# Optimization experiments

Hardware: AMD Instinct MI355X
Metric: run time of the kernel (lower is better)

## Reference

```python
import jax, jax.numpy as jnp
import numpy as np

H = 1024  # hidden size

def lstm_cell(x, h, c, Wih, Whh, b):
    # torch gate order: i, f, g, o
    g = x @ Wih.T + h @ Whh.T + b
    i, f, gg, o = jnp.split(g, 4, axis=-1)
    c = jax.nn.sigmoid(f) * c + jax.nn.sigmoid(i) * jnp.tanh(gg)
    h = jax.nn.sigmoid(o) * jnp.tanh(c)
    return h, c

def lstm_layer(x, Wih, Whh, b):
    # x: [B, S, in] -> (y [B, S, H], h_last [B, H], c_last [B, H])
    B = x.shape[0]
    h0 = jnp.zeros((B, H), x.dtype)
    def step(carry, xt):
        h, c = carry
        h, c = lstm_cell(xt, h, c, Wih, Whh, b)
        return (h, c), h
    (h, c), ys = jax.lax.scan(step, (h0, h0), jnp.swapaxes(x, 0, 1))
    return jnp.swapaxes(ys, 0, 1), h, c

def setup_inputs() -> dict:
    key = jax.random.key(0)
    ks = iter(jax.random.split(key, 24))
    V, E, B, Ss, St = 32000, 512, 32, 64, 64
    s = 0.05
    d = {
        'source': jax.random.randint(next(ks), (B, Ss), 0, V),
        'prev_outputs': jax.random.randint(next(ks), (B, St), 0, V),
        'emb': jax.random.normal(next(ks), (V, E)) * s,
        'enc_Wih0': jax.random.normal(next(ks), (4*H, E)) * s,
        'enc_Whh0': jax.random.normal(next(ks), (4*H, H)) * s,
        'enc_b0': jax.random.normal(next(ks), (4*H,)) * s,
        'enc_Wih1': jax.random.normal(next(ks), (4*H, H)) * s,
        'enc_Whh1': jax.random.normal(next(ks), (4*H, H)) * s,
        'enc_b1': jax.random.normal(next(ks), (4*H,)) * s,
        'dec_Wih0': jax.random.normal(next(ks), (4*H, E + H)) * s,
        'dec_Whh0': jax.random.normal(next(ks), (4*H, H)) * s,
        'dec_b0': jax.random.normal(next(ks), (4*H,)) * s,
        'dec_Wih1': jax.random.normal(next(ks), (4*H, H)) * s,
        'dec_Whh1': jax.random.normal(next(ks), (4*H, H)) * s,
        'dec_b1': jax.random.normal(next(ks), (4*H,)) * s,
        'Wk': jax.random.normal(next(ks), (H, H)) * s,
        'bk': jax.random.normal(next(ks), (H,)) * s,
        'Wh': jax.random.normal(next(ks), (V, H)) * s,
        'bh': jax.random.normal(next(ks), (V,)) * s,
    }
    return d

def reference(source, prev_outputs, emb, enc_Wih0, enc_Whh0, enc_b0,
              enc_Wih1, enc_Whh1, enc_b1, dec_Wih0, dec_Whh0, dec_b0,
              dec_Wih1, dec_Whh1, dec_b1, Wk, bk, Wh, bh):
    src_e = emb[source]          # [B, Ss, E]
    tgt_e = emb[prev_outputs]    # [B, St, E]
    y0, h0e, c0e = lstm_layer(src_e, enc_Wih0, enc_Whh0, enc_b0)
    enc_out, h1e, c1e = lstm_layer(y0, enc_Wih1, enc_Whh1, enc_b1)
    h = jnp.stack([h0e, h1e])    # [L, B, H]
    c = jnp.stack([c0e, c1e])
    attn_key = enc_out @ Wk.T + bk  # constant across decoder steps

    def step(carry, xt):  # xt: [B, E]
        h, c = carry
        q = h[-1]                                        # [B, H]
        scores = jnp.einsum('bh,bsh->bs', q, attn_key)   # [B, Ss]
        probs = jax.nn.softmax(scores, axis=-1)
        ctx = jnp.einsum('bs,bsh->bh', probs, enc_out)   # [B, H]
        inp = jnp.concatenate([xt, ctx], axis=-1)        # [B, E+H]
        h0n, c0n = lstm_cell(inp, h[0], c[0], dec_Wih0, dec_Whh0, dec_b0)
        h1n, c1n = lstm_cell(h0n, h[1], c[1], dec_Wih1, dec_Whh1, dec_b1)
        logits_t = h1n @ Wh.T + bh                       # [B, V]
        return (jnp.stack([h0n, h1n]), jnp.stack([c0n, c1n])), logits_t

    _, logits = jax.lax.scan(step, (h, c), jnp.swapaxes(tgt_e, 0, 1))
    return jnp.swapaxes(logits, 0, 1)  # [B, St, V]
```

## Files before the change

kernel.cpp:

```cpp
#include <hip/hip_runtime.h>
#include <cmath>

typedef short bs8 __attribute__((ext_vector_type(8)));
typedef float f32x4 __attribute__((ext_vector_type(4)));
typedef __attribute__((address_space(3))) unsigned lds_uint;
typedef __attribute__((address_space(1))) const unsigned gbl_uint;

#define NV 32000
#define SLOTH (32 * 1024)

__device__ __forceinline__ float b2f(unsigned short u) {
  union { unsigned int i; float f; } v; v.i = ((unsigned int)u) << 16; return v.f;
}
__device__ __forceinline__ unsigned short f2b(float f) {
  unsigned int u = __float_as_uint(f);
  return (unsigned short)((u + 0x7FFFu + ((u >> 16) & 1u)) >> 16);
}
__device__ __forceinline__ f32x4 mfma16(bs8 a, bs8 b, f32x4 c) {
  return __builtin_amdgcn_mfma_f32_16x16x32_bf16(a, b, c, 0, 0, 0);
}

__device__ __forceinline__ void wait16(unsigned* base, unsigned target) {
  if (threadIdx.x < 64) {
    unsigned* p = base + (threadIdx.x & 15) * 16;
    while (__hip_atomic_load(p, __ATOMIC_RELAXED, __HIP_MEMORY_SCOPE_AGENT) < target)
      __builtin_amdgcn_s_sleep(4);
  }
  __syncthreads();
}
__device__ __forceinline__ void signal16(unsigned* base, int bid) {
  __syncthreads();
  if (threadIdx.x == 0)
    __hip_atomic_fetch_add(base + (bid & 15) * 16, 1u,
                           __ATOMIC_RELAXED, __HIP_MEMORY_SCOPE_AGENT);
}

__device__ __forceinline__ void mfma_half8(
    const unsigned short* __restrict__ A, const unsigned short* __restrict__ W,
    int u0, f32x4& acc0, f32x4& acc1) {
  int tid = threadIdx.x;
  int w = tid >> 6, l = tid & 63;
  int col = l & 15;
  int kb = w * 128 + (l >> 4) * 8;
  size_t wrow = (size_t)(col >> 2) * 1024 + u0 + (col & 3);
  const unsigned short* ap = A + (size_t)col * 1024 + kb;
  const unsigned short* wp = W + wrow * 1024 + kb;
#pragma unroll
  for (int kk = 0; kk < 128; kk += 32) {
    bs8 b1 = *(const bs8*)(wp + kk);
    acc0 = mfma16(*(const bs8*)(ap + kk), b1, acc0);
    acc1 = mfma16(*(const bs8*)(ap + 16 * 1024 + kk), b1, acc1);
  }
}
__device__ __forceinline__ void red_write8(f32x4 acc0, f32x4 acc1, float (*red)[32][17]) {
  int tid = threadIdx.x;
  int w = tid >> 6, l = tid & 63, col = l & 15;
#pragma unroll
  for (int r = 0; r < 4; r++) {
    red[w][(l >> 4) * 4 + r][col] = acc0[r];
    red[w][16 + (l >> 4) * 4 + r][col] = acc1[r];
  }
  __syncthreads();
}
template <int NW, int AH>
__device__ __forceinline__ void cell_finish(
    int u0, float (*red)[32][17],
    const float* __restrict__ gxrow, const float* __restrict__ bias,
    const float* __restrict__ cprev,
    unsigned short* __restrict__ hout, float* __restrict__ cout) {
  int tid = threadIdx.x;
  if (tid < 128) {
    int b_ = tid >> 2, ul = tid & 3, u = u0 + ul;
    float s0 = 0.f, s1 = 0.f, s2 = 0.f, s3 = 0.f;
#pragma unroll
    for (int ww = 0; ww < NW; ww++) {
      s0 += red[ww][b_][ul];      s1 += red[ww][b_][4 + ul];
      s2 += red[ww][b_][8 + ul];  s3 += red[ww][b_][12 + ul];
    }
    if (gxrow) {
      const float* gp = gxrow + (size_t)b_ * 4096 + u;
      s0 += gp[0]; s1 += gp[1024]; s2 += gp[2048]; s3 += gp[3072];
    }
    if (bias) {
      s0 += bias[u]; s1 += bias[u + 1024]; s2 += bias[u + 2048]; s3 += bias[u + 3072];
    }
    float si = 1.f / (1.f + expf(-s0));
    float sf = 1.f / (1.f + expf(-s1));
    float tg = tanhf(s2);
    float so = 1.f / (1.f + expf(-s3));
    float cn = sf * cprev[b_ * 1024 + u] + si * tg;
    float hn = so * tanhf(cn);
    cout[b_ * 1024 + u] = cn;
    unsigned hv = (unsigned)f2b(hn);
    unsigned ho = __shfl_down(hv, 1);
    if (AH) {
      if (!(ul & 1)) {
        unsigned packed = hv | (ho << 16);
        __hip_atomic_store((unsigned*)hout + ((size_t)b_ * 512 + (u0 >> 1) + (ul >> 1)),
                           packed, __ATOMIC_RELAXED, __HIP_MEMORY_SCOPE_AGENT);
      }
    } else {
      hout[b_ * 1024 + u] = (unsigned short)hv;
    }
  }
}

__global__ __launch_bounds__(512) void enc_diag(
    int d,
    const unsigned short* __restrict__ wH0, const float* __restrict__ gx0,
    unsigned short* __restrict__ y0h, float* __restrict__ c0h,
    const unsigned short* __restrict__ wE1, const unsigned short* __restrict__ wH1,
    const float* __restrict__ eb1,
    unsigned short* __restrict__ y1h, float* __restrict__ c1h) {
  __shared__ float red[8][32][17];
  if (blockIdx.x < 256) {
    if (d >= 64) return;
    int u0 = blockIdx.x * 4;
    f32x4 a0 = {0.f, 0.f, 0.f, 0.f}, a1 = {0.f, 0.f, 0.f, 0.f};
    mfma_half8(y0h + (size_t)d * SLOTH, wH0, u0, a0, a1);
    red_write8(a0, a1, red);
    cell_finish<8, 0>(u0, red, gx0 + (size_t)d * 131072, nullptr,
                      c0h + (size_t)d * SLOTH,
                      y0h + (size_t)(d + 1) * SLOTH, c0h + (size_t)(d + 1) * SLOTH);
  } else {
    if (d < 1) return;
    int j = d - 1, u0 = (blockIdx.x - 256) * 4;
    f32x4 a0 = {0.f, 0.f, 0.f, 0.f}, a1 = {0.f, 0.f, 0.f, 0.f};
    mfma_half8(y0h + (size_t)(j + 1) * SLOTH, wE1, u0, a0, a1);
    mfma_half8(y1h + (size_t)j * SLOTH, wH1, u0, a0, a1);
    red_write8(a0, a1, red);
    cell_finish<8, 0>(u0, red, nullptr, eb1, c1h + (size_t)j * SLOTH,
                      y1h + (size_t)(j + 1) * SLOTH, c1h + (size_t)(j + 1) * SLOTH);
  }
}

__device__ __forceinline__ void mfma_half_lds(
    const unsigned short* __restrict__ A, const unsigned short* wl,
    f32x4& acc0, f32x4& acc1) {
  int tid = threadIdx.x;
  int w = tid >> 6, l = tid & 63;
  int col = l & 15;
  int kb = w * 256 + (l >> 4) * 8;
  const unsigned short* ap = A + (size_t)col * 1024 + kb;
  const unsigned short* wp = wl + col * 1032 + kb;
#pragma unroll
  for (int kk = 0; kk < 256; kk += 32) {
    bs8 b1 = *(const bs8*)(wp + kk);
    acc0 = mfma16(*(const bs8*)(ap + kk), b1, acc0);
    acc1 = mfma16(*(const bs8*)(ap + 16 * 1024 + kk), b1, acc1);
  }
}
__device__ __forceinline__ void red_write4(f32x4 acc0, f32x4 acc1, float (*red)[32][17]) {
  int tid = threadIdx.x;
  int w = tid >> 6, l = tid & 63, col = l & 15;
#pragma unroll
  for (int r = 0; r < 4; r++) {
    red[w][(l >> 4) * 4 + r][col] = acc0[r];
    red[w][16 + (l >> 4) * 4 + r][col] = acc1[r];
  }
  __syncthreads();
}

__global__ __launch_bounds__(256, 2) void dec_persist(
    const unsigned short* __restrict__ ak, const unsigned short* __restrict__ enc,
    const float* __restrict__ gxd,
    const unsigned short* __restrict__ wDh0, const unsigned short* __restrict__ wD0c,
    const unsigned short* __restrict__ wD1, const unsigned short* __restrict__ wDh1,
    const float* __restrict__ db1, unsigned short* __restrict__ ctxb,
    unsigned short* __restrict__ dh0, float* __restrict__ dc0,
    unsigned short* __restrict__ dh1, float* __restrict__ dc1,
    unsigned* __restrict__ flags) {
  __shared__ unsigned short wl[2][16 * 1032];
  __shared__ float red[4][32][17];
  __shared__ float qs[1024];
  __shared__ float sc[64];
  int bid = blockIdx.x, tid = threadIdx.x;
  int cell0 = (bid < 256);
  int u0 = (bid & 255) * 4;
  {
    const unsigned short* W0 = cell0 ? wDh0 : wD1;
    const unsigned short* W1 = cell0 ? wD0c : wDh1;
    for (int i = tid; i < 2048; i += 256) {
      int c = i >> 7, c8 = (i & 127) * 8;
      size_t grow = (size_t)(c >> 2) * 1024 + u0 + (c & 3);
      *(bs8*)&wl[0][c * 1032 + c8] = *(const bs8*)(W0 + grow * 1024 + c8);
      *(bs8*)&wl[1][c * 1032 + c8] = *(const bs8*)(W1 + grow * 1024 + c8);
    }
    __syncthreads();
  }
  if (cell0) {
    for (int t = 0; t < 64; t++) {
      unsigned* fP = flags + t * 768;
      unsigned* fH0 = flags + t * 768 + 256;
      if (t > 0) wait16(flags + (t - 1) * 768 + 256, 16);
      f32x4 a0 = {0.f, 0.f, 0.f, 0.f}, a1 = {0.f, 0.f, 0.f, 0.f};
      mfma_half_lds(dh0 + (size_t)t * SLOTH, wl[0], a0, a1);
      wait16(fP, 2);
      mfma_half_lds(ctxb + (size_t)t * SLOTH, wl[1], a0, a1);
      red_write4(a0, a1, red);
      cell_finish<4, 1>(u0, red, gxd + (size_t)t * 131072, nullptr,
                        dc0 + (size_t)t * SLOTH,
                        dh0 + (size_t)(t + 1) * SLOTH, dc0 + (size_t)(t + 1) * SLOTH);
      signal16(fH0, bid);
    }
  } else {
    int ab = bid - 256;
    for (int t = 0; t < 64; t++) {
      unsigned* fP = flags + t * 768;
      unsigned* fH0 = flags + t * 768 + 256;
      unsigned* fH1 = flags + t * 768 + 512;
      if (t > 0) wait16(flags + (t - 1) * 768 + 512, 16);
      if (ab < 32) {
        {
          ushort4 u4 = *(const ushort4*)(dh1 + (size_t)t * SLOTH + (size_t)ab * 1024 + tid * 4);
          qs[tid * 4 + 0] = b2f(u4.x); qs[tid * 4 + 1] = b2f(u4.y);
          qs[tid * 4 + 2] = b2f(u4.z); qs[tid * 4 + 3] = b2f(u4.w);
        }
        __syncthreads();
        int w = tid >> 6, l = tid & 63;
        for (int ss = 0; ss < 16; ss++) {
          int s = w * 16 + ss;
          const unsigned short* kr = ak + (size_t)(s * 32 + ab) * 1024;
          float p = 0.f;
#pragma unroll
          for (int i = 0; i < 4; i++) {
            int e = (l + i * 64) * 4;
            ushort4 u4 = *(const ushort4*)&kr[e];
            p += qs[e] * b2f(u4.x) + qs[e + 1] * b2f(u4.y)
               + qs[e + 2] * b2f(u4.z) + qs[e + 3] * b2f(u4.w);
          }
          for (int off = 32; off; off >>= 1) p += __shfl_down(p, off);
          if (l == 0) sc[s] = p;
        }
        __syncthreads();
        if (tid < 64) {
          float v = sc[tid], m = v;
          for (int off = 32; off; off >>= 1) m = fmaxf(m, __shfl_xor(m, off));
          float e = expf(v - m), su = e;
          for (int off = 32; off; off >>= 1) su += __shfl_xor(su, off);
          sc[tid] = e / su;
        }
        __syncthreads();
        {
          int h4 = tid * 4;
          float a0 = 0.f, a1 = 0.f, a2 = 0.f, a3 = 0.f;
#pragma unroll 8
          for (int s = 0; s < 64; s++) {
            float p = sc[s];
            ushort4 u4 = *(const ushort4*)&enc[(size_t)(s * 32 + ab) * 1024 + h4];
            a0 += p * b2f(u4.x); a1 += p * b2f(u4.y);
            a2 += p * b2f(u4.z); a3 += p * b2f(u4.w);
          }
          unsigned* cp = (unsigned*)(ctxb + (size_t)t * SLOTH) + ab * 512 + tid * 2;
          __hip_atomic_store(cp, (unsigned)f2b(a0) | ((unsigned)f2b(a1) << 16),
                             __ATOMIC_RELAXED, __HIP_MEMORY_SCOPE_AGENT);
          __hip_atomic_store(cp + 1, (unsigned)f2b(a2) | ((unsigned)f2b(a3) << 16),
                             __ATOMIC_RELAXED, __HIP_MEMORY_SCOPE_AGENT);
        }
        signal16(fP, bid);
      }
      f32x4 a0 = {0.f, 0.f, 0.f, 0.f}, a1 = {0.f, 0.f, 0.f, 0.f};
      mfma_half_lds(dh1 + (size_t)t * SLOTH, wl[1], a0, a1);
      wait16(fH0, 16);
      mfma_half_lds(dh0 + (size_t)(t + 1) * SLOTH, wl[0], a0, a1);
      red_write4(a0, a1, red);
      cell_finish<4, 1>(u0, red, nullptr, db1, dc1 + (size_t)t * SLOTH,
                        dh1 + (size_t)(t + 1) * SLOTH, dc1 + (size_t)(t + 1) * SLOTH);
      signal16(fH1, bid);
    }
  }
}

struct CvtDesc { const float* src; unsigned short* dst; int total8, cols, ld, col0, blk0; };
struct CvtArgs { CvtDesc d[11]; };
__global__ __launch_bounds__(256) void cvt_all(CvtArgs a) {
  int blk = blockIdx.x, seg = 0;
#pragma unroll
  for (int i = 1; i < 11; i++) if (blk >= a.d[i].blk0) seg = i;
  CvtDesc d = a.d[seg];
  int idx = (blk - d.blk0) * 256 + threadIdx.x;
  if (idx >= d.total8) return;
  int cpr = d.cols >> 3;
  int r = idx / cpr, c8 = (idx - r * cpr) * 8;
  const float* s = d.src + (size_t)r * d.ld + d.col0 + c8;
  float4 x = *(const float4*)s, y = *(const float4*)(s + 4);
  unsigned short o[8] = {f2b(x.x), f2b(x.y), f2b(x.z), f2b(x.w),
                         f2b(y.x), f2b(y.y), f2b(y.z), f2b(y.w)};
  *(bs8*)(d.dst + (size_t)r * d.cols + c8) = *(bs8*)o;
}

__global__ __launch_bounds__(256) void embed_kernel(
    const int* __restrict__ src, const int* __restrict__ prev,
    const float* __restrict__ emb,
    unsigned short* __restrict__ se, unsigned short* __restrict__ te) {
  int idx = blockIdx.x * 256 + threadIdx.x;
  int half = idx >> 17;
  int r = (idx >> 6) & 2047, c8 = (idx & 63) * 8;
  int s = r >> 5, b = r & 31;
  const int* tok = half ? prev : src;
  unsigned short* dst = half ? te : se;
  int t = tok[b * 64 + s];
  const float* e = emb + (size_t)t * 512 + c8;
  float4 a = *(const float4*)e, bb = *(const float4*)(e + 4);
  unsigned short o[8] = {f2b(a.x), f2b(a.y), f2b(a.z), f2b(a.w),
                         f2b(bb.x), f2b(bb.y), f2b(bb.z), f2b(bb.w)};
  *(bs8*)(dst + (size_t)r * 512 + c8) = *(bs8*)o;
}

#define NFLAGS 49152
__global__ __launch_bounds__(256) void zero_init(
    unsigned short* y0h, unsigned short* y1h, float* c0h, float* c1h,
    unsigned* flags) {
  int i = blockIdx.x * 256 + threadIdx.x;
  y0h[i] = 0; y1h[i] = 0; c0h[i] = 0.f; c1h[i] = 0.f;
  for (int j = i; j < NFLAGS; j += 32768) flags[j] = 0u;
}
__global__ __launch_bounds__(256) void init_dec(
    const unsigned short* __restrict__ y0f, const unsigned short* __restrict__ y1f,
    const float* __restrict__ c0f, const float* __restrict__ c1f,
    unsigned short* dh0, unsigned short* dh1, float* dc0, float* dc1) {
  int i = blockIdx.x * 256 + threadIdx.x;
  dh0[i] = y0f[i]; dh1[i] = y1f[i]; dc0[i] = c0f[i]; dc1[i] = c1f[i];
}

template <int OUTMODE>
__global__ __launch_bounds__(256) void gemm_bf16(
    const unsigned short* __restrict__ A, int lda,
    const unsigned short* __restrict__ B, int ldb,
    const float* __restrict__ bias, void* __restrict__ Cp, int ldc, int K) {
  __shared__ unsigned short As[128 * 64];
  __shared__ unsigned short Bs[128 * 64];
  int tid = threadIdx.x;
  int m0, n0;
  if (OUTMODE == 1) {
    int nwg = gridDim.x * gridDim.y;
    int orig = blockIdx.y * gridDim.x + blockIdx.x;
    int q = nwg >> 3;
    int wg = (orig & 7) * q + (orig >> 3);
    m0 = (wg % gridDim.x) * 128;
    n0 = (wg / gridDim.x) * 128;
  } else {
    m0 = blockIdx.x * 128; n0 = blockIdx.y * 128;
  }
  int w = tid >> 6, l = tid & 63;
  int wr = w >> 1, wc = w & 1;
  int swz = ((l & 7) * 8) ^ ((l >> 3) * 8);
  f32x4 acc[4][4];
#pragma unroll
  for (int i = 0; i < 4; i++)
#pragma unroll
    for (int j = 0; j < 4; j++)
#pragma unroll
      for (int r = 0; r < 4; r++) acc[i][j][r] = 0.f;

  for (int k0 = 0; k0 < K; k0 += 64) {
    __syncthreads();
#pragma unroll
    for (int i = 0; i < 4; i++) {
      int rb = w * 8 + i * 32;
      const unsigned short* ga = A + (size_t)(m0 + rb + (l >> 3)) * lda + k0 + swz;
      __builtin_amdgcn_global_load_lds((gbl_uint*)ga, (lds_uint*)&As[rb * 64], 16, 0, 0);
      const unsigned short* gb = B + (size_t)(n0 + rb + (l >> 3)) * ldb + k0 + swz;
      __builtin_amdgcn_global_load_lds((gbl_uint*)gb, (lds_uint*)&Bs[rb * 64], 16, 0, 0);
    }
    __syncthreads();
#pragma unroll
    for (int kk = 0; kk < 2; kk++) {
      bs8 af[4], bfr[4];
#pragma unroll
      for (int i = 0; i < 4; i++) {
        int R = wr * 64 + i * 16 + (l & 15);
        af[i] = *(const bs8*)&As[R * 64 + ((kk * 32 + (l >> 4) * 8) ^ ((R & 7) * 8))];
      }
#pragma unroll
      for (int j = 0; j < 4; j++) {
        int R = wc * 64 + j * 16 + (l & 15);
        bfr[j] = *(const bs8*)&Bs[R * 64 + ((kk * 32 + (l >> 4) * 8) ^ ((R & 7) * 8))];
      }
#pragma unroll
      for (int i = 0; i < 4; i++)
#pragma unroll
        for (int j = 0; j < 4; j++)
          acc[i][j] = mfma16(af[i], bfr[j], acc[i][j]);
    }
  }
#pragma unroll
  for (int i = 0; i < 4; i++) {
    int mrow = m0 + wr * 64 + i * 16 + (l >> 4) * 4;
#pragma unroll
    for (int j = 0; j < 4; j++) {
      int n = n0 + wc * 64 + j * 16 + (l & 15);
      float bb = bias ? bias[n] : 0.f;
#pragma unroll
      for (int r = 0; r < 4; r++) {
        int m = mrow + r;
        float v = acc[i][j][r] + bb;
        if (OUTMODE == 1)
          ((float*)Cp)[(size_t)(m & 31) * (64ull * NV) + (size_t)(m >> 5) * NV + n] = v;
        else if (OUTMODE == 2)
          ((unsigned short*)Cp)[(size_t)m * ldc + n] = f2b(v);
        else
          ((float*)Cp)[(size_t)m * ldc + n] = v;
      }
    }
  }
}

extern "C" void kernel_launch(void* const* d_in, const int* in_sizes, int n_in,
                              void* d_out, int out_size, void* d_ws, size_t ws_size,
                              hipStream_t stream) {
  (void)in_sizes; (void)n_in; (void)out_size; (void)ws_size;
  const int*   src   = (const int*)d_in[0];
  const int*   prev  = (const int*)d_in[1];
  const float* emb   = (const float*)d_in[2];
  const float* eWih0 = (const float*)d_in[3];
  const float* eWhh0 = (const float*)d_in[4];
  const float* eb0   = (const float*)d_in[5];
  const float* eWih1 = (const float*)d_in[6];
  const float* eWhh1 = (const float*)d_in[7];
  const float* eb1   = (const float*)d_in[8];
  const float* dWih0 = (const float*)d_in[9];
  const float* dWhh0 = (const float*)d_in[10];
  const float* db0   = (const float*)d_in[11];
  const float* dWih1 = (const float*)d_in[12];
  const float* dWhh1 = (const float*)d_in[13];
  const float* db1   = (const float*)d_in[14];
  const float* Wk    = (const float*)d_in[15];
  const float* bk    = (const float*)d_in[16];
  const float* Wh    = (const float*)d_in[17];
  const float* bh    = (const float*)d_in[18];
  float* out = (float*)d_out;

  char* p = (char*)d_ws;
  auto alloc = [&](size_t bytes) {
    char* r = p; p += (bytes + 255) & ~(size_t)255; return r;
  };
  float* gx0 = (float*)alloc(2048ull * 4096 * 4);
  float* gxd = (float*)alloc(2048ull * 4096 * 4);
  float* c0h = (float*)alloc(65ull * SLOTH * 4);
  float* c1h = (float*)alloc(65ull * SLOTH * 4);
  float* dc0 = (float*)alloc(65ull * SLOTH * 4);
  float* dc1 = (float*)alloc(65ull * SLOTH * 4);
  unsigned short* y0h  = (unsigned short*)alloc(65ull * SLOTH * 2);
  unsigned short* y1h  = (unsigned short*)alloc(65ull * SLOTH * 2);
  unsigned short* dh0  = (unsigned short*)alloc(65ull * SLOTH * 2);
  unsigned short* dh1  = (unsigned short*)alloc(65ull * SLOTH * 2);
  unsigned short* ctxb = (unsigned short*)alloc(64ull * SLOTH * 2);
  unsigned short* se   = (unsigned short*)alloc(2048ull * 512 * 2);
  unsigned short* te   = (unsigned short*)alloc(2048ull * 512 * 2);
  unsigned short* ak   = (unsigned short*)alloc(2048ull * 1024 * 2);
  unsigned short* wE0  = (unsigned short*)alloc(4096ull * 512 * 2);
  unsigned short* wH0  = (unsigned short*)alloc(4096ull * 1024 * 2);
  unsigned short* wE1  = (unsigned short*)alloc(4096ull * 1024 * 2);
  unsigned short* wH1  = (unsigned short*)alloc(4096ull * 1024 * 2);
  unsigned short* wD0x = (unsigned short*)alloc(4096ull * 512 * 2);
  unsigned short* wD0c = (unsigned short*)alloc(4096ull * 1024 * 2);
  unsigned short* wDh0 = (unsigned short*)alloc(4096ull * 1024 * 2);
  unsigned short* wD1  = (unsigned short*)alloc(4096ull * 1024 * 2);
  unsigned short* wDh1 = (unsigned short*)alloc(4096ull * 1024 * 2);
  unsigned short* wK   = (unsigned short*)alloc(1024ull * 1024 * 2);
  unsigned short* wV   = (unsigned short*)alloc((size_t)NV * 1024 * 2);
  unsigned* flags = (unsigned*)alloc((size_t)NFLAGS * 4);

  CvtArgs ca; int nb = 0, ci = 0;
  auto addcvt = [&](const float* s, unsigned short* d, int rows, int cols, int ld, int c0) {
    int t8 = rows * cols / 8;
    ca.d[ci++] = CvtDesc{s, d, t8, cols, ld, c0, nb};
    nb += (t8 + 255) / 256;
  };
  addcvt(eWih0, wE0, 4096, 512, 512, 0);
  addcvt(eWhh0, wH0, 4096, 1024, 1024, 0);
  addcvt(eWih1, wE1, 4096, 1024, 1024, 0);
  addcvt(eWhh1, wH1, 4096, 1024, 1024, 0);
  addcvt(dWih0, wD0x, 4096, 512, 1536, 0);
  addcvt(dWih0, wD0c, 4096, 1024, 1536, 512);
  addcvt(dWhh0, wDh0, 4096, 1024, 1024, 0);
  addcvt(dWih1, wD1, 4096, 1024, 1024, 0);
  addcvt(dWhh1, wDh1, 4096, 1024, 1024, 0);
  addcvt(Wk, wK, 1024, 1024, 1024, 0);
  addcvt(Wh, wV, NV, 1024, 1024, 0);
  cvt_all<<<nb, 256, 0, stream>>>(ca);

  zero_init<<<128, 256, 0, stream>>>(y0h, y1h, c0h, c1h, flags);
  embed_kernel<<<1024, 256, 0, stream>>>(src, prev, emb, se, te);

  gemm_bf16<0><<<dim3(16, 32), 256, 0, stream>>>(se, 512, wE0, 512, eb0, gx0, 4096, 512);
  gemm_bf16<0><<<dim3(16, 32), 256, 0, stream>>>(te, 512, wD0x, 512, db0, gxd, 4096, 512);

  for (int d = 0; d <= 64; d++)
    enc_diag<<<512, 512, 0, stream>>>(d, wH0, gx0, y0h, c0h, wE1, wH1, eb1, y1h, c1h);

  gemm_bf16<2><<<dim3(16, 8), 256, 0, stream>>>(y1h + SLOTH, 1024, wK, 1024, bk, ak, 1024, 1024);
  init_dec<<<128, 256, 0, stream>>>(y0h + 64 * SLOTH, y1h + 64 * SLOTH,
                                    c0h + 64 * SLOTH, c1h + 64 * SLOTH,
                                    dh0, dh1, dc0, dc1);
  dec_persist<<<512, 256, 0, stream>>>(ak, y1h + SLOTH, gxd, wDh0, wD0c, wD1, wDh1,
                                       db1, ctxb, dh0, dc0, dh1, dc1, flags);
  gemm_bf16<1><<<dim3(16, 250), 256, 0, stream>>>(dh1 + SLOTH, 1024, wV, 1024, bh, out, NV, 1024);
}
```

Before: 2.975 ms.

## Replace atomic-counter barriers with per-block epoch flags in decoder persistent kernel

```diff
diff --git a/kernel.cpp b/kernel.cpp
--- a/kernel.cpp
+++ b/kernel.cpp
@@ -20,19 +20,30 @@
   return __builtin_amdgcn_mfma_f32_16x16x32_bf16(a, b, c, 0, 0, 0);
 }
 
-__device__ __forceinline__ void wait16(unsigned* base, unsigned target) {
+__device__ __forceinline__ void waitN(const unsigned* slots, int n, unsigned target) {
   if (threadIdx.x < 64) {
-    unsigned* p = base + (threadIdx.x & 15) * 16;
-    while (__hip_atomic_load(p, __ATOMIC_RELAXED, __HIP_MEMORY_SCOPE_AGENT) < target)
-      __builtin_amdgcn_s_sleep(4);
+    for (;;) {
+      unsigned mn = 0xffffffffu;
+      for (int i = threadIdx.x; i < n; i += 64) {
+        unsigned v = __hip_atomic_load(slots + (size_t)i * 4,
+                                       __ATOMIC_RELAXED, __HIP_MEMORY_SCOPE_AGENT);
+        mn = mn < v ? mn : v;
+      }
+#pragma unroll
+      for (int off = 32; off; off >>= 1) {
+        unsigned o = __shfl_xor(mn, off);
+        mn = mn < o ? mn : o;
+      }
+      if (mn >= target) break;
+      __builtin_amdgcn_s_sleep(2);
+    }
   }
   __syncthreads();
 }
-__device__ __forceinline__ void signal16(unsigned* base, int bid) {
+__device__ __forceinline__ void signal_slot(unsigned* slot, unsigned val) {
   __syncthreads();
   if (threadIdx.x == 0)
-    __hip_atomic_fetch_add(base + (bid & 15) * 16, 1u,
-                           __ATOMIC_RELAXED, __HIP_MEMORY_SCOPE_AGENT);
+    __hip_atomic_store(slot, val, __ATOMIC_RELAXED, __HIP_MEMORY_SCOPE_AGENT);
 }
 
 __device__ __forceinline__ void mfma_half8(
@@ -177,6 +188,9 @@
   int bid = blockIdx.x, tid = threadIdx.x;
   int cell0 = (bid < 256);
   int u0 = (bid & 255) * 4;
+  unsigned* fH0 = flags;
+  unsigned* fH1 = flags + 1024;
+  unsigned* fP  = flags + 2048;
   {
     const unsigned short* W0 = cell0 ? wDh0 : wD1;
     const unsigned short* W1 = cell0 ? wD0c : wDh1;
@@ -190,26 +204,21 @@
   }
   if (cell0) {
     for (int t = 0; t < 64; t++) {
-      unsigned* fP = flags + t * 768;
-      unsigned* fH0 = flags + t * 768 + 256;
-      if (t > 0) wait16(flags + (t - 1) * 768 + 256, 16);
+      if (t > 0) waitN(fH0, 256, (unsigned)t);
       f32x4 a0 = {0.f, 0.f, 0.f, 0.f}, a1 = {0.f, 0.f, 0.f, 0.f};
       mfma_half_lds(dh0 + (size_t)t * SLOTH, wl[0], a0, a1);
-      wait16(fP, 2);
+      waitN(fP, 32, (unsigned)(t + 1));
       mfma_half_lds(ctxb + (size_t)t * SLOTH, wl[1], a0, a1);
       red_write4(a0, a1, red);
       cell_finish<4, 1>(u0, red, gxd + (size_t)t * 131072, nullptr,
                         dc0 + (size_t)t * SLOTH,
                         dh0 + (size_t)(t + 1) * SLOTH, dc0 + (size_t)(t + 1) * SLOTH);
-      signal16(fH0, bid);
+      signal_slot(fH0 + (size_t)bid * 4, (unsigned)(t + 1));
     }
   } else {
     int ab = bid - 256;
     for (int t = 0; t < 64; t++) {
-      unsigned* fP = flags + t * 768;
-      unsigned* fH0 = flags + t * 768 + 256;
-      unsigned* fH1 = flags + t * 768 + 512;
-      if (t > 0) wait16(flags + (t - 1) * 768 + 512, 16);
+      if (t > 0) waitN(fH1, 256, (unsigned)t);
       if (ab < 32) {
         {
           ushort4 u4 = *(const ushort4*)(dh1 + (size_t)t * SLOTH + (size_t)ab * 1024 + tid * 4);
@@ -257,16 +266,16 @@
           __hip_atomic_store(cp + 1, (unsigned)f2b(a2) | ((unsigned)f2b(a3) << 16),
                              __ATOMIC_RELAXED, __HIP_MEMORY_SCOPE_AGENT);
         }
-        signal16(fP, bid);
+        signal_slot(fP + (size_t)ab * 4, (unsigned)(t + 1));
       }
       f32x4 a0 = {0.f, 0.f, 0.f, 0.f}, a1 = {0.f, 0.f, 0.f, 0.f};
       mfma_half_lds(dh1 + (size_t)t * SLOTH, wl[1], a0, a1);
-      wait16(fH0, 16);
+      waitN(fH0, 256, (unsigned)(t + 1));
       mfma_half_lds(dh0 + (size_t)(t + 1) * SLOTH, wl[0], a0, a1);
       red_write4(a0, a1, red);
       cell_finish<4, 1>(u0, red, nullptr, db1, dc1 + (size_t)t * SLOTH,
                         dh1 + (size_t)(t + 1) * SLOTH, dc1 + (size_t)(t + 1) * SLOTH);
-      signal16(fH1, bid);
+      signal_slot(fH1 + (size_t)(bid - 256) * 4, (unsigned)(t + 1));
     }
   }
 }
@@ -307,13 +316,13 @@
   *(bs8*)(dst + (size_t)r * 512 + c8) = *(bs8*)o;
 }
 
-#define NFLAGS 49152
+#define NFLAGS 4096
 __global__ __launch_bounds__(256) void zero_init(
     unsigned short* y0h, unsigned short* y1h, float* c0h, float* c1h,
     unsigned* flags) {
   int i = blockIdx.x * 256 + threadIdx.x;
   y0h[i] = 0; y1h[i] = 0; c0h[i] = 0.f; c1h[i] = 0.f;
-  for (int j = i; j < NFLAGS; j += 32768) flags[j] = 0u;
+  if (i < NFLAGS) flags[i] = 0u;
 }
 __global__ __launch_bounds__(256) void init_dec(
     const unsigned short* __restrict__ y0f, const unsigned short* __restrict__ y1f,
```

Result: faster. 2.800 ms (-5.9%).
